# Kernel tuning notes

Measured on AMD Instinct MI355X. Metric: run time of the kernel, lower is better.

The kernel has to match this reference:

```python
import jax, jax.numpy as jnp
import numpy as np
from jax import lax

# dims
B, T = 64, 1024
ANNOT, RNN, MEM, ATTN = 512, 1024, 512, 512
FILTERS, KSIZE = 32, 31
PAD = (KSIZE - 1) // 2  # 15, SAME padding


def setup_inputs() -> dict:
    key = jax.random.key(0)
    ks = jax.random.split(key, 20)
    s = 0.02
    return {
        "memory": jax.random.normal(ks[0], (B, MEM), jnp.float32),
        "context": jax.random.normal(ks[1], (B, ANNOT), jnp.float32),
        "rnn_state": jax.random.normal(ks[2], (B, RNN), jnp.float32),
        "annots": jax.random.normal(ks[3], (B, T, ANNOT), jnp.float32),
        "atten": jax.random.uniform(ks[4], (B, 2, T), jnp.float32),
        "mask": jnp.ones((B, T), jnp.int32),
        "t": 0,
        # GRUCell params (torch gate order: r, z, n)
        "W_ih": jax.random.normal(ks[5], (3 * RNN, ANNOT + MEM), jnp.float32) * s,
        "W_hh": jax.random.normal(ks[6], (3 * RNN, RNN), jnp.float32) * s,
        "b_ih": jnp.zeros((3 * RNN,), jnp.float32),
        "b_hh": jnp.zeros((3 * RNN,), jnp.float32),
        # location-sensitive attention params
        "conv_w": jax.random.normal(ks[7], (FILTERS, 2, KSIZE), jnp.float32) * s,
        "loc_w": jax.random.normal(ks[8], (ATTN, FILTERS), jnp.float32) * s,
        "loc_b": jnp.zeros((ATTN,), jnp.float32),
        "q_w": jax.random.normal(ks[9], (ATTN, RNN), jnp.float32) * s,
        "q_b": jnp.zeros((ATTN,), jnp.float32),
        "a_w": jax.random.normal(ks[10], (ATTN, ANNOT), jnp.float32) * s,
        "a_b": jnp.zeros((ATTN,), jnp.float32),
        "v_w": jax.random.normal(ks[11], (1, ATTN), jnp.float32) * s,
    }


def _gru_cell(x, h, W_ih, W_hh, b_ih, b_hh):
    gi = x @ W_ih.T + b_ih  # [B, 3H]
    gh = h @ W_hh.T + b_hh
    i_r, i_z, i_n = jnp.split(gi, 3, axis=-1)
    h_r, h_z, h_n = jnp.split(gh, 3, axis=-1)
    r = jax.nn.sigmoid(i_r + h_r)
    z = jax.nn.sigmoid(i_z + h_z)
    n = jnp.tanh(i_n + r * h_n)
    return (1.0 - z) * n + z * h


def reference(memory, context, rnn_state, annots, atten, mask, t,
              W_ih, W_hh, b_ih, b_hh, conv_w, loc_w, loc_b,
              q_w, q_b, a_w, a_b, v_w):
    # GRU step on [memory; prev_context]
    rnn_input = jnp.concatenate([memory, context], axis=-1)  # [B, MEM+ANNOT]
    rnn_output = _gru_cell(rnn_input, rnn_state, W_ih, W_hh, b_ih, b_hh)  # [B, RNN]

    # location features: SAME conv over [B, 2, T] -> [B, FILTERS, T]
    loc_conv = lax.conv_general_dilated(
        atten, conv_w, window_strides=(1,), padding=[(PAD, PAD)],
        dimension_numbers=("NCH", "OIH", "NCH"))
    processed_loc = jnp.einsum("bft,af->bta", loc_conv, loc_w) + loc_b  # [B,T,ATTN]

    processed_query = (rnn_output @ q_w.T + q_b)[:, None, :]            # [B,1,ATTN]
    processed_annots = jnp.einsum("btd,ad->bta", annots, a_w) + a_b     # [B,T,ATTN]

    energy = jnp.tanh(processed_query + processed_annots + processed_loc)
    alignment = jnp.einsum("bta,a->bt", energy, v_w[0])                 # [B,T]

    # mask fill with -inf where mask == 0
    alignment = jnp.where(mask == 0, -jnp.inf, alignment)

    # sigmoid-normalized attention weights
    sig = jax.nn.sigmoid(alignment)
    alignment = sig / jnp.sum(sig, axis=1, keepdims=True)               # [B,T]

    new_context = jnp.einsum("bt,btd->bd", alignment, annots)           # [B,ANNOT]
    return rnn_output, new_context, alignment
```

## Files before the change

kernel.cpp:

```cpp
#include <hip/hip_runtime.h>

typedef float f32x4 __attribute__((ext_vector_type(4)));
typedef short bf16x8 __attribute__((ext_vector_type(8)));

__device__ __forceinline__ unsigned int pk2(float a, float b) {
    unsigned int ua = __float_as_uint(a); ua += 0x7FFFu + ((ua >> 16) & 1u);
    unsigned int ub = __float_as_uint(b); ub += 0x7FFFu + ((ub >> 16) & 1u);
    return __builtin_amdgcn_perm(ub, ua, 0x07060302u);
}
__device__ __forceinline__ unsigned short bf16_rne(float a) {
    unsigned int ua = __float_as_uint(a);
    ua += 0x7FFFu + ((ua >> 16) & 1u);
    return (unsigned short)(ua >> 16);
}
__device__ __forceinline__ float tanh_fast(float x) {
    float e = __expf(x + x);
    return 1.f - 2.f / (e + 1.f);
}
__device__ __forceinline__ f32x4 mfma16(bf16x8 a, bf16x8 b, f32x4 c) {
    return __builtin_amdgcn_mfma_f32_16x16x32_bf16(a, b, c, 0, 0, 0);
}

#define Q_WIH   786432
#define Q_WHH   1572864
#define Q_QW    1703936
#define Q_X2    1720320
#define Q_X1    1736704
#define Q_BAW   1802240
#define Q_BLW   1806336
#define Q_EB    1806464

__global__ __launch_bounds__(256) void k_convert(
    const float* __restrict__ Wih, const float* __restrict__ Whh,
    const float* __restrict__ qw, const float* __restrict__ rnn_state,
    const float* __restrict__ memory, const float* __restrict__ context,
    const float* __restrict__ aw, const float* __restrict__ lw,
    const float* __restrict__ ab, const float* __restrict__ lb,
    unsigned short* __restrict__ Wihb, unsigned short* __restrict__ Whhb,
    unsigned short* __restrict__ qwb, unsigned short* __restrict__ X2b,
    unsigned short* __restrict__ X1b, unsigned short* __restrict__ Bbig,
    float* __restrict__ ebias)
{
    int q = blockIdx.x * 256 + threadIdx.x;
    if (q >= Q_EB) return;
    if (q < Q_WIH) {
        int i = q * 4;
        float4 v = *(const float4*)(Wih + i);
        uint2 u; u.x = pk2(v.x, v.y); u.y = pk2(v.z, v.w);
        *(uint2*)(Wihb + i) = u;
    } else if (q < Q_WHH) {
        int i = (q - Q_WIH) * 4;
        float4 v = *(const float4*)(Whh + i);
        uint2 u; u.x = pk2(v.x, v.y); u.y = pk2(v.z, v.w);
        *(uint2*)(Whhb + i) = u;
    } else if (q < Q_QW) {
        int i = (q - Q_WHH) * 4;
        float4 v = *(const float4*)(qw + i);
        uint2 u; u.x = pk2(v.x, v.y); u.y = pk2(v.z, v.w);
        *(uint2*)(qwb + i) = u;
    } else if (q < Q_X2) {
        int i = (q - Q_QW) * 4;
        float4 v = *(const float4*)(rnn_state + i);
        uint2 u; u.x = pk2(v.x, v.y); u.y = pk2(v.z, v.w);
        *(uint2*)(X2b + i) = u;
    } else if (q < Q_X1) {
        int i = (q - Q_X2) * 4;
        int b = i >> 10, c = i & 1023;
        const float* s = (c < 512) ? (memory + b * 512 + c) : (context + b * 512 + (c - 512));
        float4 v = *(const float4*)s;
        uint2 u; u.x = pk2(v.x, v.y); u.y = pk2(v.z, v.w);
        *(uint2*)(X1b + i) = u;
    } else if (q < Q_BAW) {
        int i = (q - Q_X1) * 4;
        int a = i >> 9, c = i & 511;
        float4 v = *(const float4*)(aw + a * 512 + c);
        uint2 u; u.x = pk2(v.x, v.y); u.y = pk2(v.z, v.w);
        *(uint2*)(Bbig + a * 544 + c) = u;
    } else if (q < Q_BLW) {
        int i = (q - Q_BAW) * 4;
        int a = i >> 5, c = i & 31;
        float4 v = *(const float4*)(lw + a * 32 + c);
        uint2 u; u.x = pk2(v.x, v.y); u.y = pk2(v.z, v.w);
        *(uint2*)(Bbig + a * 544 + 512 + c) = u;
    } else {
        int i = (q - Q_BLW) * 4;
        float4 va = *(const float4*)(ab + i);
        float4 vb = *(const float4*)(lb + i);
        float4 r; r.x = va.x + vb.x; r.y = va.y + vb.y; r.z = va.z + vb.z; r.w = va.w + vb.w;
        *(float4*)(ebias + i) = r;
    }
}

__global__ __launch_bounds__(256) void k_conv(
    const float* __restrict__ atten, const float* __restrict__ convw,
    unsigned short* __restrict__ Lconv)
{
    __shared__ float att_s[2 * 160];
    __shared__ float cw_s[1984];
    const int b = blockIdx.x >> 3;
    const int tbase = (blockIdx.x & 7) * 128;
    const int tid = threadIdx.x;
    for (int i = tid; i < 320; i += 256) {
        int c = i / 160, j = i % 160;
        float v = 0.f;
        int pos = tbase - 15 + j;
        if (j < 158 && pos >= 0 && pos < 1024) v = atten[b * 2048 + c * 1024 + pos];
        att_s[c * 160 + j] = v;
    }
    for (int i = tid; i < 1984; i += 256) cw_s[i] = convw[i];
    __syncthreads();
    const int f = tid & 31, tq = tid >> 5;
    float acc[16];
#pragma unroll
    for (int i = 0; i < 16; ++i) acc[i] = 0.f;
    for (int c = 0; c < 2; ++c) {
        for (int k = 0; k < 31; ++k) {
            float w = cw_s[f * 62 + c * 31 + k];
            int base = c * 160 + tq * 16 + k;
#pragma unroll
            for (int ti = 0; ti < 16; ++ti) acc[ti] += w * att_s[base + ti];
        }
    }
#pragma unroll
    for (int ti = 0; ti < 16; ++ti) {
        int t = tbase + tq * 16 + ti;
        Lconv[(b * 1024 + t) * 32 + f] = bf16_rne(acc[ti]);
    }
}

__global__ __launch_bounds__(256, 2) void k_gemm128(
    const unsigned short* __restrict__ A1, const unsigned short* __restrict__ A2,
    const unsigned short* __restrict__ B1, const unsigned short* __restrict__ B2,
    const float* __restrict__ bias1, const float* __restrict__ bias2,
    float* __restrict__ C, int N, int n_split, int K)
{
    __shared__ __align__(16) unsigned short As[128 * 32];
    __shared__ __align__(16) unsigned short Bs[128 * 32];
    const int tid = threadIdx.x;
    const int nBase = blockIdx.x * 128;
    const bool use2 = nBase >= n_split;
    const unsigned short* A = use2 ? A2 : A1;
    const unsigned short* Bp = use2 ? B2 : B1;
    const float* bias = use2 ? bias2 : bias1;
    const int boff = use2 ? n_split : 0;

    const int lane = tid & 63, wave = tid >> 6;
    const int wrow = wave >> 1, wcol = wave & 1;
    const int c = lane & 15, qd = lane >> 4;
    const int sr = tid >> 2, sk = (tid & 3) * 8;

    { uint4 z = {0u, 0u, 0u, 0u}; *(uint4*)&As[(64 + sr) * 32 + sk] = z; }

    const f32x4 fz = {0.f, 0.f, 0.f, 0.f};
    f32x4 acc[4][4];
#pragma unroll
    for (int i = 0; i < 4; ++i)
#pragma unroll
        for (int j = 0; j < 4; ++j) acc[i][j] = fz;

    const int nk = K >> 5;
    for (int kc = 0; kc < nk; ++kc) {
        const int k0 = kc * 32;
        *(uint4*)&As[sr * 32 + sk] = *(const uint4*)&A[sr * K + k0 + sk];
        *(uint4*)&Bs[sr * 32 + sk] = *(const uint4*)&Bp[(nBase - boff + sr) * K + k0 + sk];
        *(uint4*)&Bs[(sr + 64) * 32 + sk] = *(const uint4*)&Bp[(nBase - boff + sr + 64) * K + k0 + sk];
        __syncthreads();
        bf16x8 af[4], bfr[4];
#pragma unroll
        for (int i = 0; i < 4; ++i) af[i] = *(const bf16x8*)&As[(wrow * 64 + i * 16 + c) * 32 + qd * 8];
#pragma unroll
        for (int j = 0; j < 4; ++j) bfr[j] = *(const bf16x8*)&Bs[(wcol * 64 + j * 16 + c) * 32 + qd * 8];
#pragma unroll
        for (int i = 0; i < 4; ++i)
#pragma unroll
            for (int j = 0; j < 4; ++j) acc[i][j] = mfma16(af[i], bfr[j], acc[i][j]);
        __syncthreads();
    }
#pragma unroll
    for (int i = 0; i < 4; ++i)
#pragma unroll
        for (int r = 0; r < 4; ++r) {
            int row = wrow * 64 + i * 16 + qd * 4 + r;
            if (row < 64) {
#pragma unroll
                for (int j = 0; j < 4; ++j) {
                    int col = nBase + wcol * 64 + j * 16 + c;
                    C[row * N + col] = acc[i][j][r] + bias[col - boff];
                }
            }
        }
}

__global__ __launch_bounds__(256) void k_gates(
    const float* __restrict__ Cg, const float* __restrict__ h0,
    float* __restrict__ outv, unsigned short* __restrict__ X3b)
{
    int idx = blockIdx.x * 256 + threadIdx.x;
    int b = idx >> 10, h = idx & 1023;
    const float* g = Cg + b * 6144;
    float ir = g[h], iz = g[h + 1024], inn = g[h + 2048];
    float hr = g[h + 3072], hz = g[h + 4096], hn = g[h + 5120];
    float r = 1.f / (1.f + __expf(-(ir + hr)));
    float z = 1.f / (1.f + __expf(-(iz + hz)));
    float n = tanh_fast(inn + r * hn);
    float o = (1.f - z) * n + z * h0[idx];
    outv[idx] = o;
    X3b[idx] = bf16_rne(o);
}

__global__ __launch_bounds__(256, 2) void k_attn(
    const float* __restrict__ annots, const unsigned short* __restrict__ Lconv,
    const unsigned short* __restrict__ Bbig, const float* __restrict__ pqm,
    const float* __restrict__ ebias, const float* __restrict__ vw,
    float* __restrict__ wsal)
{
    __shared__ __align__(16) unsigned short As[128 * 32];
    __shared__ __align__(16) unsigned short Bs[128 * 32];
    __shared__ float red[2][128];
    const int tid = threadIdx.x;
    const int nblk = blockIdx.x & 3;
    const int mblk = blockIdx.x >> 2;
    const int btBase = mblk * 128;
    const int nBase = nblk * 128;
    const int b = btBase >> 10;
    const float* pqb = pqm + b * 512;

    const int lane = tid & 63, wave = tid >> 6;
    const int wrow = wave >> 1, wcol = wave & 1;
    const int c = lane & 15, qd = lane >> 4;
    const int sr = tid >> 2, sk = (tid & 3) * 8;

    const f32x4 fz = {0.f, 0.f, 0.f, 0.f};
    f32x4 acc[4][4];
#pragma unroll
    for (int i = 0; i < 4; ++i)
#pragma unroll
        for (int j = 0; j < 4; ++j) acc[i][j] = fz;

    for (int kc = 0; kc < 17; ++kc) {
        const int k0 = kc * 32;
        if (kc < 16) {
            const float* p0 = annots + (long)(btBase + sr) * 512 + k0 + sk;
            float4 v0 = *(const float4*)p0;
            float4 v1 = *(const float4*)(p0 + 4);
            uint4 u;
            u.x = pk2(v0.x, v0.y); u.y = pk2(v0.z, v0.w);
            u.z = pk2(v1.x, v1.y); u.w = pk2(v1.z, v1.w);
            *(uint4*)&As[sr * 32 + sk] = u;
            const float* p1 = p0 + 64 * 512;
            v0 = *(const float4*)p1;
            v1 = *(const float4*)(p1 + 4);
            uint4 u2;
            u2.x = pk2(v0.x, v0.y); u2.y = pk2(v0.z, v0.w);
            u2.z = pk2(v1.x, v1.y); u2.w = pk2(v1.z, v1.w);
            *(uint4*)&As[(sr + 64) * 32 + sk] = u2;
        } else {
            *(uint4*)&As[sr * 32 + sk] = *(const uint4*)&Lconv[(btBase + sr) * 32 + sk];
            *(uint4*)&As[(sr + 64) * 32 + sk] = *(const uint4*)&Lconv[(btBase + 64 + sr) * 32 + sk];
        }
        *(uint4*)&Bs[sr * 32 + sk] = *(const uint4*)&Bbig[(nBase + sr) * 544 + k0 + sk];
        *(uint4*)&Bs[(sr + 64) * 32 + sk] = *(const uint4*)&Bbig[(nBase + 64 + sr) * 544 + k0 + sk];
        __syncthreads();
        bf16x8 af[4], bfr[4];
#pragma unroll
        for (int i = 0; i < 4; ++i) af[i] = *(const bf16x8*)&As[(wrow * 64 + i * 16 + c) * 32 + qd * 8];
#pragma unroll
        for (int j = 0; j < 4; ++j) bfr[j] = *(const bf16x8*)&Bs[(wcol * 64 + j * 16 + c) * 32 + qd * 8];
#pragma unroll
        for (int i = 0; i < 4; ++i)
#pragma unroll
            for (int j = 0; j < 4; ++j) acc[i][j] = mfma16(af[i], bfr[j], acc[i][j]);
        __syncthreads();
    }
    float pe[4], vv[4];
#pragma unroll
    for (int j = 0; j < 4; ++j) {
        int colg = nBase + wcol * 64 + j * 16 + c;
        pe[j] = pqb[colg] + ebias[colg];
        vv[j] = vw[colg];
    }
#pragma unroll
    for (int i = 0; i < 4; ++i)
#pragma unroll
        for (int r = 0; r < 4; ++r) {
            float p = 0.f;
#pragma unroll
            for (int j = 0; j < 4; ++j) {
                float e = tanh_fast(acc[i][j][r] + pe[j]);
                p += vv[j] * e;
            }
            p += __shfl_xor(p, 1);
            p += __shfl_xor(p, 2);
            p += __shfl_xor(p, 4);
            p += __shfl_xor(p, 8);
            if (c == 0) red[wcol][wrow * 64 + i * 16 + qd * 4 + r] = p;
        }
    __syncthreads();
    if (tid < 128) wsal[nblk * 65536 + btBase + tid] = red[0][tid] + red[1][tid];
}

__global__ __launch_bounds__(256) void k_ctx(
    const float* __restrict__ annots, const float* __restrict__ wsal,
    const int* __restrict__ mask, float* __restrict__ out)
{
    __shared__ float al[1024];
    __shared__ float wsum[4];
    __shared__ float red[256];
    const int b = blockIdx.x >> 3;
    const int chunk = blockIdx.x & 7;
    const int tid = threadIdx.x;
    float lsum = 0.f;
#pragma unroll
    for (int p = 0; p < 4; ++p) {
        int t = p * 256 + tid;
        int bt = b * 1024 + t;
        float raw = wsal[bt] + wsal[65536 + bt] + wsal[131072 + bt] + wsal[196608 + bt];
        float s = (mask[bt] != 0) ? 1.f / (1.f + __expf(-raw)) : 0.f;
        al[t] = s;
        lsum += s;
    }
    for (int off = 32; off > 0; off >>= 1) lsum += __shfl_xor(lsum, off);
    if ((tid & 63) == 0) wsum[tid >> 6] = lsum;
    __syncthreads();
    const float tot = wsum[0] + wsum[1] + wsum[2] + wsum[3];
    const float inv = 1.f / tot;
    if (chunk == 0) {
#pragma unroll
        for (int p = 0; p < 4; ++p) {
            int t = p * 256 + tid;
            out[98304 + b * 1024 + t] = al[t] * inv;
        }
    }
    const int dq = tid & 63, tq = tid >> 6;
    const int d = chunk * 64 + dq;
    const float* ap = annots + (long)(b * 1024 + tq * 256) * 512 + d;
    float acc = 0.f;
#pragma unroll 4
    for (int t = 0; t < 256; ++t) acc += al[tq * 256 + t] * ap[(long)t * 512];
    red[tid] = acc;
    __syncthreads();
    if (tid < 64) {
        float s2 = red[tid] + red[64 + tid] + red[128 + tid] + red[192 + tid];
        out[65536 + b * 512 + chunk * 64 + tid] = s2 * inv;
    }
}

extern "C" void kernel_launch(void* const* d_in, const int* in_sizes, int n_in,
                              void* d_out, int out_size, void* d_ws, size_t ws_size,
                              hipStream_t stream) {
    const float* memory    = (const float*)d_in[0];
    const float* context   = (const float*)d_in[1];
    const float* rnn_state = (const float*)d_in[2];
    const float* annots    = (const float*)d_in[3];
    const float* atten     = (const float*)d_in[4];
    const int*   mask      = (const int*)d_in[5];
    const float* W_ih   = (const float*)d_in[7];
    const float* W_hh   = (const float*)d_in[8];
    const float* b_ih   = (const float*)d_in[9];
    const float* b_hh   = (const float*)d_in[10];
    const float* conv_w = (const float*)d_in[11];
    const float* loc_w  = (const float*)d_in[12];
    const float* loc_b  = (const float*)d_in[13];
    const float* q_w    = (const float*)d_in[14];
    const float* q_b    = (const float*)d_in[15];
    const float* a_w    = (const float*)d_in[16];
    const float* a_b    = (const float*)d_in[17];
    const float* v_w    = (const float*)d_in[18];
    float* out = (float*)d_out;

    char* w8 = (char*)d_ws;
    unsigned short* Lconv = (unsigned short*)(w8 + 0);
    unsigned short* Bbig  = (unsigned short*)(w8 + 4194304);
    unsigned short* Wihb  = (unsigned short*)(w8 + 4751360);
    unsigned short* Whhb  = (unsigned short*)(w8 + 11042816);
    unsigned short* qwb   = (unsigned short*)(w8 + 17334272);
    unsigned short* X1b   = (unsigned short*)(w8 + 18382848);
    unsigned short* X2b   = (unsigned short*)(w8 + 18513920);
    unsigned short* X3b   = (unsigned short*)(w8 + 18644992);
    float*          Cgru  = (float*)(w8 + 18776064);
    float*          pq    = (float*)(w8 + 20348928);
    float*          ebias = (float*)(w8 + 20480000);
    float*          wsal  = (float*)(w8 + 20482048);

    k_convert<<<7057, 256, 0, stream>>>(W_ih, W_hh, q_w, rnn_state, memory, context,
                                        a_w, loc_w, a_b, loc_b,
                                        Wihb, Whhb, qwb, X2b, X1b, Bbig, ebias);
    k_conv<<<512, 256, 0, stream>>>(atten, conv_w, Lconv);
    k_gemm128<<<48, 256, 0, stream>>>(X1b, X2b, Wihb, Whhb, b_ih, b_hh,
                                      Cgru, 6144, 3072, 1024);
    k_gates<<<256, 256, 0, stream>>>(Cgru, rnn_state, out, X3b);
    k_gemm128<<<4, 256, 0, stream>>>(X3b, X3b, qwb, qwb, q_b, q_b,
                                     pq, 512, 0x40000000, 1024);
    k_attn<<<2048, 256, 0, stream>>>(annots, Lconv, Bbig, pq, ebias, v_w, wsal);
    k_ctx<<<512, 256, 0, stream>>>(annots, wsal, mask, out);
}
```

Before: 385.1 us.

## Widen attention GEMM tile to full N, split-K small GEMMs, fuse prep kernels

The attention-energy kernel now computes all 512 attention columns per 64-row block, so each annotation row is read and converted to bf16 once instead of once per column block. The B weights are loaded with direct global-to-LDS loads into an XOR-swizzled layout. The GRU and query GEMMs switch to a split-K kernel with 64-row A tiles, which doubles the block count, and bias adds move into the consumers. The convert and conv kernels merge into one launch. The trade-off is larger LDS use and more accumulator registers per block in the attention kernel, which may lower occupancy.

```diff
diff --git a/kernel.cpp b/kernel.cpp
--- a/kernel.cpp
+++ b/kernel.cpp
@@ -19,6 +19,11 @@
 }
 __device__ __forceinline__ f32x4 mfma16(bf16x8 a, bf16x8 b, f32x4 c) {
     return __builtin_amdgcn_mfma_f32_16x16x32_bf16(a, b, c, 0, 0, 0);
+}
+__device__ __forceinline__ void ald16(const void* g, void* l) {
+    __builtin_amdgcn_global_load_lds(
+        (const __attribute__((address_space(1))) unsigned int*)g,
+        (__attribute__((address_space(3))) unsigned int*)l, 16, 0, 0);
 }
 
 #define Q_WIH   786432
@@ -29,177 +34,179 @@
 #define Q_BAW   1802240
 #define Q_BLW   1806336
 #define Q_EB    1806464
-
-__global__ __launch_bounds__(256) void k_convert(
+#define NCVT    7057
+
+__global__ __launch_bounds__(256) void k_prep(
     const float* __restrict__ Wih, const float* __restrict__ Whh,
     const float* __restrict__ qw, const float* __restrict__ rnn_state,
     const float* __restrict__ memory, const float* __restrict__ context,
     const float* __restrict__ aw, const float* __restrict__ lw,
     const float* __restrict__ ab, const float* __restrict__ lb,
+    const float* __restrict__ atten, const float* __restrict__ convw,
     unsigned short* __restrict__ Wihb, unsigned short* __restrict__ Whhb,
     unsigned short* __restrict__ qwb, unsigned short* __restrict__ X2b,
     unsigned short* __restrict__ X1b, unsigned short* __restrict__ Bbig,
-    float* __restrict__ ebias)
-{
-    int q = blockIdx.x * 256 + threadIdx.x;
-    if (q >= Q_EB) return;
-    if (q < Q_WIH) {
-        int i = q * 4;
-        float4 v = *(const float4*)(Wih + i);
-        uint2 u; u.x = pk2(v.x, v.y); u.y = pk2(v.z, v.w);
-        *(uint2*)(Wihb + i) = u;
-    } else if (q < Q_WHH) {
-        int i = (q - Q_WIH) * 4;
-        float4 v = *(const float4*)(Whh + i);
-        uint2 u; u.x = pk2(v.x, v.y); u.y = pk2(v.z, v.w);
-        *(uint2*)(Whhb + i) = u;
-    } else if (q < Q_QW) {
-        int i = (q - Q_WHH) * 4;
-        float4 v = *(const float4*)(qw + i);
-        uint2 u; u.x = pk2(v.x, v.y); u.y = pk2(v.z, v.w);
-        *(uint2*)(qwb + i) = u;
-    } else if (q < Q_X2) {
-        int i = (q - Q_QW) * 4;
-        float4 v = *(const float4*)(rnn_state + i);
-        uint2 u; u.x = pk2(v.x, v.y); u.y = pk2(v.z, v.w);
-        *(uint2*)(X2b + i) = u;
-    } else if (q < Q_X1) {
-        int i = (q - Q_X2) * 4;
-        int b = i >> 10, c = i & 1023;
-        const float* s = (c < 512) ? (memory + b * 512 + c) : (context + b * 512 + (c - 512));
-        float4 v = *(const float4*)s;
-        uint2 u; u.x = pk2(v.x, v.y); u.y = pk2(v.z, v.w);
-        *(uint2*)(X1b + i) = u;
-    } else if (q < Q_BAW) {
-        int i = (q - Q_X1) * 4;
-        int a = i >> 9, c = i & 511;
-        float4 v = *(const float4*)(aw + a * 512 + c);
-        uint2 u; u.x = pk2(v.x, v.y); u.y = pk2(v.z, v.w);
-        *(uint2*)(Bbig + a * 544 + c) = u;
-    } else if (q < Q_BLW) {
-        int i = (q - Q_BAW) * 4;
-        int a = i >> 5, c = i & 31;
-        float4 v = *(const float4*)(lw + a * 32 + c);
-        uint2 u; u.x = pk2(v.x, v.y); u.y = pk2(v.z, v.w);
-        *(uint2*)(Bbig + a * 544 + 512 + c) = u;
-    } else {
-        int i = (q - Q_BLW) * 4;
-        float4 va = *(const float4*)(ab + i);
-        float4 vb = *(const float4*)(lb + i);
-        float4 r; r.x = va.x + vb.x; r.y = va.y + vb.y; r.z = va.z + vb.z; r.w = va.w + vb.w;
-        *(float4*)(ebias + i) = r;
-    }
-}
-
-__global__ __launch_bounds__(256) void k_conv(
-    const float* __restrict__ atten, const float* __restrict__ convw,
-    unsigned short* __restrict__ Lconv)
+    float* __restrict__ ebias, unsigned short* __restrict__ Lconv)
 {
     __shared__ float att_s[2 * 160];
     __shared__ float cw_s[1984];
-    const int b = blockIdx.x >> 3;
-    const int tbase = (blockIdx.x & 7) * 128;
     const int tid = threadIdx.x;
-    for (int i = tid; i < 320; i += 256) {
-        int c = i / 160, j = i % 160;
-        float v = 0.f;
-        int pos = tbase - 15 + j;
-        if (j < 158 && pos >= 0 && pos < 1024) v = atten[b * 2048 + c * 1024 + pos];
-        att_s[c * 160 + j] = v;
-    }
-    for (int i = tid; i < 1984; i += 256) cw_s[i] = convw[i];
-    __syncthreads();
-    const int f = tid & 31, tq = tid >> 5;
-    float acc[16];
-#pragma unroll
-    for (int i = 0; i < 16; ++i) acc[i] = 0.f;
-    for (int c = 0; c < 2; ++c) {
-        for (int k = 0; k < 31; ++k) {
-            float w = cw_s[f * 62 + c * 31 + k];
-            int base = c * 160 + tq * 16 + k;
-#pragma unroll
-            for (int ti = 0; ti < 16; ++ti) acc[ti] += w * att_s[base + ti];
-        }
-    }
-#pragma unroll
-    for (int ti = 0; ti < 16; ++ti) {
-        int t = tbase + tq * 16 + ti;
-        Lconv[(b * 1024 + t) * 32 + f] = bf16_rne(acc[ti]);
-    }
-}
-
-__global__ __launch_bounds__(256, 2) void k_gemm128(
+    if (blockIdx.x < NCVT) {
+        int q = blockIdx.x * 256 + tid;
+        if (q >= Q_EB) return;
+        if (q < Q_WIH) {
+            int i = q * 4;
+            float4 v = *(const float4*)(Wih + i);
+            uint2 u; u.x = pk2(v.x, v.y); u.y = pk2(v.z, v.w);
+            *(uint2*)(Wihb + i) = u;
+        } else if (q < Q_WHH) {
+            int i = (q - Q_WIH) * 4;
+            float4 v = *(const float4*)(Whh + i);
+            uint2 u; u.x = pk2(v.x, v.y); u.y = pk2(v.z, v.w);
+            *(uint2*)(Whhb + i) = u;
+        } else if (q < Q_QW) {
+            int i = (q - Q_WHH) * 4;
+            float4 v = *(const float4*)(qw + i);
+            uint2 u; u.x = pk2(v.x, v.y); u.y = pk2(v.z, v.w);
+            *(uint2*)(qwb + i) = u;
+        } else if (q < Q_X2) {
+            int i = (q - Q_QW) * 4;
+            float4 v = *(const float4*)(rnn_state + i);
+            uint2 u; u.x = pk2(v.x, v.y); u.y = pk2(v.z, v.w);
+            *(uint2*)(X2b + i) = u;
+        } else if (q < Q_X1) {
+            int i = (q - Q_X2) * 4;
+            int b = i >> 10, c = i & 1023;
+            const float* s = (c < 512) ? (memory + b * 512 + c) : (context + b * 512 + (c - 512));
+            float4 v = *(const float4*)s;
+            uint2 u; u.x = pk2(v.x, v.y); u.y = pk2(v.z, v.w);
+            *(uint2*)(X1b + i) = u;
+        } else if (q < Q_BAW) {
+            int i = (q - Q_X1) * 4;
+            int a = i >> 9, c = i & 511;
+            float4 v = *(const float4*)(aw + a * 512 + c);
+            uint2 u; u.x = pk2(v.x, v.y); u.y = pk2(v.z, v.w);
+            *(uint2*)(Bbig + a * 544 + c) = u;
+        } else if (q < Q_BLW) {
+            int i = (q - Q_BAW) * 4;
+            int a = i >> 5, c = i & 31;
+            float4 v = *(const float4*)(lw + a * 32 + c);
+            uint2 u; u.x = pk2(v.x, v.y); u.y = pk2(v.z, v.w);
+            *(uint2*)(Bbig + a * 544 + 512 + c) = u;
+        } else {
+            int i = (q - Q_BLW) * 4;
+            float4 va = *(const float4*)(ab + i);
+            float4 vb = *(const float4*)(lb + i);
+            float4 r; r.x = va.x + vb.x; r.y = va.y + vb.y; r.z = va.z + vb.z; r.w = va.w + vb.w;
+            *(float4*)(ebias + i) = r;
+        }
+    } else {
+        const int bid = blockIdx.x - NCVT;
+        const int b = bid >> 3;
+        const int tbase = (bid & 7) * 128;
+        for (int i = tid; i < 320; i += 256) {
+            int c = i / 160, j = i % 160;
+            float v = 0.f;
+            int pos = tbase - 15 + j;
+            if (j < 158 && pos >= 0 && pos < 1024) v = atten[b * 2048 + c * 1024 + pos];
+            att_s[c * 160 + j] = v;
+        }
+        for (int i = tid; i < 1984; i += 256) cw_s[i] = convw[i];
+        __syncthreads();
+        const int f = tid & 31, tq = tid >> 5;
+        float acc[16];
+#pragma unroll
+        for (int i = 0; i < 16; ++i) acc[i] = 0.f;
+        for (int c = 0; c < 2; ++c) {
+            for (int k = 0; k < 31; ++k) {
+                float w = cw_s[f * 62 + c * 31 + k];
+                int base = c * 160 + tq * 16 + k;
+#pragma unroll
+                for (int ti = 0; ti < 16; ++ti) acc[ti] += w * att_s[base + ti];
+            }
+        }
+#pragma unroll
+        for (int ti = 0; ti < 16; ++ti) {
+            int t = tbase + tq * 16 + ti;
+            Lconv[(b * 1024 + t) * 32 + f] = bf16_rne(acc[ti]);
+        }
+    }
+}
+
+__global__ __launch_bounds__(256, 4) void k_gemm_ks(
     const unsigned short* __restrict__ A1, const unsigned short* __restrict__ A2,
     const unsigned short* __restrict__ B1, const unsigned short* __restrict__ B2,
-    const float* __restrict__ bias1, const float* __restrict__ bias2,
-    float* __restrict__ C, int N, int n_split, int K)
-{
-    __shared__ __align__(16) unsigned short As[128 * 32];
+    float* __restrict__ C, int N, int nTiles, int n_split, int K, int Klen)
+{
+    __shared__ __align__(16) unsigned short As[64 * 32];
     __shared__ __align__(16) unsigned short Bs[128 * 32];
     const int tid = threadIdx.x;
-    const int nBase = blockIdx.x * 128;
+    const int nb = blockIdx.x % nTiles;
+    const int ks = blockIdx.x / nTiles;
+    const int nBase = nb * 128;
     const bool use2 = nBase >= n_split;
     const unsigned short* A = use2 ? A2 : A1;
-    const unsigned short* Bp = use2 ? B2 : B1;
-    const float* bias = use2 ? bias2 : bias1;
-    const int boff = use2 ? n_split : 0;
-
-    const int lane = tid & 63, wave = tid >> 6;
-    const int wrow = wave >> 1, wcol = wave & 1;
+    const unsigned short* B = use2 ? B2 : B1;
+    const int brow0 = nBase - (use2 ? n_split : 0);
+    const int lane = tid & 63, w = tid >> 6;
     const int c = lane & 15, qd = lane >> 4;
-    const int sr = tid >> 2, sk = (tid & 3) * 8;
-
-    { uint4 z = {0u, 0u, 0u, 0u}; *(uint4*)&As[(64 + sr) * 32 + sk] = z; }
+    const int lr = lane >> 2;
+    const int swzl = ((lane & 3) ^ ((lr >> 1) & 3)) * 8;
 
     const f32x4 fz = {0.f, 0.f, 0.f, 0.f};
-    f32x4 acc[4][4];
+    f32x4 acc[4][2];
+#pragma unroll
+    for (int i = 0; i < 4; ++i) { acc[i][0] = fz; acc[i][1] = fz; }
+
+    const int k0b = ks * Klen;
+    const int nkc = Klen >> 5;
+    for (int kc = 0; kc < nkc; ++kc) {
+        const int k0 = k0b + kc * 32;
+        ald16(A + (size_t)(w * 16 + lr) * K + k0 + swzl, &As[w * 512]);
+        ald16(B + (size_t)(brow0 + w * 16 + lr) * K + k0 + swzl, &Bs[w * 512]);
+        ald16(B + (size_t)(brow0 + 64 + w * 16 + lr) * K + k0 + swzl, &Bs[2048 + w * 512]);
+        __syncthreads();
+        const int rdoff = (qd ^ ((c >> 1) & 3)) * 8;
+        bf16x8 af[4];
+#pragma unroll
+        for (int i = 0; i < 4; ++i) af[i] = *(const bf16x8*)&As[(i * 16 + c) * 32 + rdoff];
+#pragma unroll
+        for (int j = 0; j < 2; ++j) {
+            bf16x8 bj = *(const bf16x8*)&Bs[(w * 32 + j * 16 + c) * 32 + rdoff];
+#pragma unroll
+            for (int i = 0; i < 4; ++i) acc[i][j] = mfma16(af[i], bj, acc[i][j]);
+        }
+        __syncthreads();
+    }
+    float* Cp = C + (size_t)ks * 64 * N;
 #pragma unroll
     for (int i = 0; i < 4; ++i)
 #pragma unroll
-        for (int j = 0; j < 4; ++j) acc[i][j] = fz;
-
-    const int nk = K >> 5;
-    for (int kc = 0; kc < nk; ++kc) {
-        const int k0 = kc * 32;
-        *(uint4*)&As[sr * 32 + sk] = *(const uint4*)&A[sr * K + k0 + sk];
-        *(uint4*)&Bs[sr * 32 + sk] = *(const uint4*)&Bp[(nBase - boff + sr) * K + k0 + sk];
-        *(uint4*)&Bs[(sr + 64) * 32 + sk] = *(const uint4*)&Bp[(nBase - boff + sr + 64) * K + k0 + sk];
-        __syncthreads();
-        bf16x8 af[4], bfr[4];
-#pragma unroll
-        for (int i = 0; i < 4; ++i) af[i] = *(const bf16x8*)&As[(wrow * 64 + i * 16 + c) * 32 + qd * 8];
-#pragma unroll
-        for (int j = 0; j < 4; ++j) bfr[j] = *(const bf16x8*)&Bs[(wcol * 64 + j * 16 + c) * 32 + qd * 8];
-#pragma unroll
-        for (int i = 0; i < 4; ++i)
-#pragma unroll
-            for (int j = 0; j < 4; ++j) acc[i][j] = mfma16(af[i], bfr[j], acc[i][j]);
-        __syncthreads();
-    }
-#pragma unroll
-    for (int i = 0; i < 4; ++i)
-#pragma unroll
         for (int r = 0; r < 4; ++r) {
-            int row = wrow * 64 + i * 16 + qd * 4 + r;
-            if (row < 64) {
-#pragma unroll
-                for (int j = 0; j < 4; ++j) {
-                    int col = nBase + wcol * 64 + j * 16 + c;
-                    C[row * N + col] = acc[i][j][r] + bias[col - boff];
-                }
+            int row = i * 16 + qd * 4 + r;
+#pragma unroll
+            for (int j = 0; j < 2; ++j) {
+                int col = nBase + w * 32 + j * 16 + c;
+                Cp[row * N + col] = acc[i][j][r];
             }
         }
 }
 
 __global__ __launch_bounds__(256) void k_gates(
     const float* __restrict__ Cg, const float* __restrict__ h0,
+    const float* __restrict__ bih, const float* __restrict__ bhh,
     float* __restrict__ outv, unsigned short* __restrict__ X3b)
 {
     int idx = blockIdx.x * 256 + threadIdx.x;
     int b = idx >> 10, h = idx & 1023;
-    const float* g = Cg + b * 6144;
-    float ir = g[h], iz = g[h + 1024], inn = g[h + 2048];
-    float hr = g[h + 3072], hz = g[h + 4096], hn = g[h + 5120];
+    const float* g0 = Cg + b * 6144;
+    const float* g1 = Cg + 393216 + b * 6144;
+    float ir = g0[h] + g1[h] + bih[h];
+    float iz = g0[h + 1024] + g1[h + 1024] + bih[h + 1024];
+    float inn = g0[h + 2048] + g1[h + 2048] + bih[h + 2048];
+    float hr = g0[h + 3072] + g1[h + 3072] + bhh[h];
+    float hz = g0[h + 4096] + g1[h + 4096] + bhh[h + 1024];
+    float hn = g0[h + 5120] + g1[h + 5120] + bhh[h + 2048];
     float r = 1.f / (1.f + __expf(-(ir + hr)));
     float z = 1.f / (1.f + __expf(-(iz + hz)));
     float n = tanh_fast(inn + r * hn);
@@ -210,73 +217,65 @@
 
 __global__ __launch_bounds__(256, 2) void k_attn(
     const float* __restrict__ annots, const unsigned short* __restrict__ Lconv,
-    const unsigned short* __restrict__ Bbig, const float* __restrict__ pqm,
-    const float* __restrict__ ebias, const float* __restrict__ vw,
-    float* __restrict__ wsal)
-{
-    __shared__ __align__(16) unsigned short As[128 * 32];
-    __shared__ __align__(16) unsigned short Bs[128 * 32];
-    __shared__ float red[2][128];
+    const unsigned short* __restrict__ Bbig, const float* __restrict__ pqP,
+    const float* __restrict__ qb, const float* __restrict__ ebias,
+    const float* __restrict__ vw, float* __restrict__ wsal)
+{
+    __shared__ __align__(16) unsigned short As[64 * 32];
+    __shared__ __align__(16) unsigned short Bs[512 * 32];
+    __shared__ float red[4][64];
     const int tid = threadIdx.x;
-    const int nblk = blockIdx.x & 3;
-    const int mblk = blockIdx.x >> 2;
-    const int btBase = mblk * 128;
-    const int nBase = nblk * 128;
+    const int btBase = blockIdx.x * 64;
     const int b = btBase >> 10;
-    const float* pqb = pqm + b * 512;
-
-    const int lane = tid & 63, wave = tid >> 6;
-    const int wrow = wave >> 1, wcol = wave & 1;
+    const int lane = tid & 63, w = tid >> 6;
     const int c = lane & 15, qd = lane >> 4;
-    const int sr = tid >> 2, sk = (tid & 3) * 8;
+    const int lr = lane >> 2;
+    const int swzl = ((lane & 3) ^ ((lr >> 1) & 3)) * 8;
+    const int arow = tid >> 2, alc = tid & 3;
+    const int apofs = (alc ^ ((arow >> 1) & 3)) * 8;
 
     const f32x4 fz = {0.f, 0.f, 0.f, 0.f};
-    f32x4 acc[4][4];
+    f32x4 acc[4][8];
 #pragma unroll
     for (int i = 0; i < 4; ++i)
 #pragma unroll
-        for (int j = 0; j < 4; ++j) acc[i][j] = fz;
+        for (int j = 0; j < 8; ++j) acc[i][j] = fz;
 
     for (int kc = 0; kc < 17; ++kc) {
         const int k0 = kc * 32;
+#pragma unroll
+        for (int s = 0; s < 8; ++s)
+            ald16(Bbig + (size_t)(s * 64 + w * 16 + lr) * 544 + k0 + swzl,
+                  &Bs[s * 2048 + w * 512]);
         if (kc < 16) {
-            const float* p0 = annots + (long)(btBase + sr) * 512 + k0 + sk;
-            float4 v0 = *(const float4*)p0;
-            float4 v1 = *(const float4*)(p0 + 4);
+            const float* p = annots + (size_t)(btBase + arow) * 512 + k0 + alc * 8;
+            float4 v0 = *(const float4*)p;
+            float4 v1 = *(const float4*)(p + 4);
             uint4 u;
             u.x = pk2(v0.x, v0.y); u.y = pk2(v0.z, v0.w);
             u.z = pk2(v1.x, v1.y); u.w = pk2(v1.z, v1.w);
-            *(uint4*)&As[sr * 32 + sk] = u;
-            const float* p1 = p0 + 64 * 512;
-            v0 = *(const float4*)p1;
-            v1 = *(const float4*)(p1 + 4);
-            uint4 u2;
-            u2.x = pk2(v0.x, v0.y); u2.y = pk2(v0.z, v0.w);
-            u2.z = pk2(v1.x, v1.y); u2.w = pk2(v1.z, v1.w);
-            *(uint4*)&As[(sr + 64) * 32 + sk] = u2;
+            *(uint4*)&As[arow * 32 + apofs] = u;
         } else {
-            *(uint4*)&As[sr * 32 + sk] = *(const uint4*)&Lconv[(btBase + sr) * 32 + sk];
-            *(uint4*)&As[(sr + 64) * 32 + sk] = *(const uint4*)&Lconv[(btBase + 64 + sr) * 32 + sk];
-        }
-        *(uint4*)&Bs[sr * 32 + sk] = *(const uint4*)&Bbig[(nBase + sr) * 544 + k0 + sk];
-        *(uint4*)&Bs[(sr + 64) * 32 + sk] = *(const uint4*)&Bbig[(nBase + 64 + sr) * 544 + k0 + sk];
-        __syncthreads();
-        bf16x8 af[4], bfr[4];
-#pragma unroll
-        for (int i = 0; i < 4; ++i) af[i] = *(const bf16x8*)&As[(wrow * 64 + i * 16 + c) * 32 + qd * 8];
-#pragma unroll
-        for (int j = 0; j < 4; ++j) bfr[j] = *(const bf16x8*)&Bs[(wcol * 64 + j * 16 + c) * 32 + qd * 8];
-#pragma unroll
-        for (int i = 0; i < 4; ++i)
-#pragma unroll
-            for (int j = 0; j < 4; ++j) acc[i][j] = mfma16(af[i], bfr[j], acc[i][j]);
-        __syncthreads();
-    }
-    float pe[4], vv[4];
-#pragma unroll
-    for (int j = 0; j < 4; ++j) {
-        int colg = nBase + wcol * 64 + j * 16 + c;
-        pe[j] = pqb[colg] + ebias[colg];
+            ald16(Lconv + (size_t)(btBase + w * 16 + lr) * 32 + swzl, &As[w * 512]);
+        }
+        __syncthreads();
+        const int rdoff = (qd ^ ((c >> 1) & 3)) * 8;
+        bf16x8 af[4];
+#pragma unroll
+        for (int i = 0; i < 4; ++i) af[i] = *(const bf16x8*)&As[(i * 16 + c) * 32 + rdoff];
+#pragma unroll
+        for (int j = 0; j < 8; ++j) {
+            bf16x8 bj = *(const bf16x8*)&Bs[(w * 128 + j * 16 + c) * 32 + rdoff];
+#pragma unroll
+            for (int i = 0; i < 4; ++i) acc[i][j] = mfma16(af[i], bj, acc[i][j]);
+        }
+        __syncthreads();
+    }
+    float pe[8], vv[8];
+#pragma unroll
+    for (int j = 0; j < 8; ++j) {
+        int colg = w * 128 + j * 16 + c;
+        pe[j] = pqP[b * 512 + colg] + pqP[32768 + b * 512 + colg] + qb[colg] + ebias[colg];
         vv[j] = vw[colg];
     }
 #pragma unroll
@@ -285,18 +284,17 @@
         for (int r = 0; r < 4; ++r) {
             float p = 0.f;
 #pragma unroll
-            for (int j = 0; j < 4; ++j) {
-                float e = tanh_fast(acc[i][j][r] + pe[j]);
-                p += vv[j] * e;
-            }
+            for (int j = 0; j < 8; ++j)
+                p += vv[j] * tanh_fast(acc[i][j][r] + pe[j]);
             p += __shfl_xor(p, 1);
             p += __shfl_xor(p, 2);
             p += __shfl_xor(p, 4);
             p += __shfl_xor(p, 8);
-            if (c == 0) red[wcol][wrow * 64 + i * 16 + qd * 4 + r] = p;
+            if (c == 0) red[w][i * 16 + qd * 4 + r] = p;
         }
     __syncthreads();
-    if (tid < 128) wsal[nblk * 65536 + btBase + tid] = red[0][tid] + red[1][tid];
+    if (tid < 64)
+        wsal[btBase + tid] = red[0][tid] + red[1][tid] + red[2][tid] + red[3][tid];
 }
 
 __global__ __launch_bounds__(256) void k_ctx(
@@ -314,7 +312,7 @@
     for (int p = 0; p < 4; ++p) {
         int t = p * 256 + tid;
         int bt = b * 1024 + t;
-        float raw = wsal[bt] + wsal[65536 + bt] + wsal[131072 + bt] + wsal[196608 + bt];
+        float raw = wsal[bt];
         float s = (mask[bt] != 0) ? 1.f / (1.f + __expf(-raw)) : 0.f;
         al[t] = s;
         lsum += s;
@@ -333,10 +331,10 @@
     }
     const int dq = tid & 63, tq = tid >> 6;
     const int d = chunk * 64 + dq;
-    const float* ap = annots + (long)(b * 1024 + tq * 256) * 512 + d;
+    const float* ap = annots + (size_t)(b * 1024 + tq * 256) * 512 + d;
     float acc = 0.f;
 #pragma unroll 4
-    for (int t = 0; t < 256; ++t) acc += al[tq * 256 + t] * ap[(long)t * 512];
+    for (int t = 0; t < 256; ++t) acc += al[tq * 256 + t] * ap[(size_t)t * 512];
     red[tid] = acc;
     __syncthreads();
     if (tid < 64) {
@@ -378,19 +376,16 @@
     unsigned short* X2b   = (unsigned short*)(w8 + 18513920);
     unsigned short* X3b   = (unsigned short*)(w8 + 18644992);
     float*          Cgru  = (float*)(w8 + 18776064);
-    float*          pq    = (float*)(w8 + 20348928);
-    float*          ebias = (float*)(w8 + 20480000);
-    float*          wsal  = (float*)(w8 + 20482048);
-
-    k_convert<<<7057, 256, 0, stream>>>(W_ih, W_hh, q_w, rnn_state, memory, context,
-                                        a_w, loc_w, a_b, loc_b,
-                                        Wihb, Whhb, qwb, X2b, X1b, Bbig, ebias);
-    k_conv<<<512, 256, 0, stream>>>(atten, conv_w, Lconv);
-    k_gemm128<<<48, 256, 0, stream>>>(X1b, X2b, Wihb, Whhb, b_ih, b_hh,
-                                      Cgru, 6144, 3072, 1024);
-    k_gates<<<256, 256, 0, stream>>>(Cgru, rnn_state, out, X3b);
-    k_gemm128<<<4, 256, 0, stream>>>(X3b, X3b, qwb, qwb, q_b, q_b,
-                                     pq, 512, 0x40000000, 1024);
-    k_attn<<<2048, 256, 0, stream>>>(annots, Lconv, Bbig, pq, ebias, v_w, wsal);
+    float*          pqP   = (float*)(w8 + 18776064);
+    float*          wsal  = (float*)(w8 + 19038208);
+    float*          ebias = (float*)(w8 + 21921792);
+
+    k_prep<<<NCVT + 512, 256, 0, stream>>>(W_ih, W_hh, q_w, rnn_state, memory, context,
+                                           a_w, loc_w, a_b, loc_b, atten, conv_w,
+                                           Wihb, Whhb, qwb, X2b, X1b, Bbig, ebias, Lconv);
+    k_gemm_ks<<<96, 256, 0, stream>>>(X1b, X2b, Wihb, Whhb, Cgru, 6144, 48, 3072, 1024, 512);
+    k_gates<<<256, 256, 0, stream>>>(Cgru, rnn_state, b_ih, b_hh, out, X3b);
+    k_gemm_ks<<<8, 256, 0, stream>>>(X3b, X3b, qwb, qwb, pqP, 512, 4, 0x40000000, 1024, 512);
+    k_attn<<<1024, 256, 0, stream>>>(annots, Lconv, Bbig, pqP, q_b, ebias, v_w, wsal);
     k_ctx<<<512, 256, 0, stream>>>(annots, wsal, mask, out);
 }
```

Measured after the change: 345.8 us. 1.11x faster.
